# Kernel optimization log

Hardware: AMD Instinct MI355X
Metric: run time of the kernel (lower is better)

## Reference

```python
import jax, jax.numpy as jnp
import numpy as np


def _lap(cost):
    """Jonker-Volgenant / e-maxx O(n^3) Hungarian on a square numpy cost matrix.
    Returns col_of_row[r] = column optimally assigned to row r (same optimum as
    scipy.optimize.linear_sum_assignment). 1-indexed internals per the classic
    formulation; inner column scans are numpy-vectorized."""
    n = cost.shape[0]
    u = np.zeros(n + 1, dtype=np.float64)
    v = np.zeros(n + 1, dtype=np.float64)
    p = np.zeros(n + 1, dtype=np.int64)    # p[j] = row matched to column j (0 = none)
    way = np.zeros(n + 1, dtype=np.int64)
    for i in range(1, n + 1):
        p[0] = i
        j0 = 0
        minv = np.full(n + 1, np.inf)
        used = np.zeros(n + 1, dtype=bool)
        while True:
            used[j0] = True
            i0 = p[j0]
            cur = cost[i0 - 1].astype(np.float64) - u[i0] - v[1:]
            free = ~used[1:]
            mv = minv[1:]          # view into minv
            wy = way[1:]           # view into way
            better = free & (cur < mv)
            mv[better] = cur[better]
            wy[better] = j0
            cand = np.where(free, mv, np.inf)
            j1 = int(np.argmin(cand)) + 1
            delta = cand[j1 - 1]
            u[p[used]] += delta
            v[used] -= delta
            mv[free] -= delta
            j0 = j1
            if p[j0] == 0:
                break
        while j0:
            j1 = way[j0]
            p[j0] = p[j1]
            j0 = j1
    col_of_row = np.empty(n, dtype=np.int64)
    for j in range(1, n + 1):
        col_of_row[p[j] - 1] = j - 1
    return col_of_row


def setup_inputs() -> dict:
    key = jax.random.key(0)
    k1, k2 = jax.random.split(key)
    pred = jax.random.normal(k1, (32, 256, 2), dtype=jnp.float32)
    target = jax.random.normal(k2, (32, 256, 2), dtype=jnp.float32)
    return {"pred": pred, "target": target}


def reference(pred, target):
    B = pred.shape[0]
    p = pred.reshape(B, -1, 2).astype(jnp.float32)   # [B, N, 2]
    t = target.reshape(B, -1, 2).astype(jnp.float32)  # [B, N, 2]
    # batched euclidean cdist: [B, N, N]
    dist = jnp.sqrt(jnp.sum((p[:, :, None, :] - t[:, None, :, :]) ** 2, axis=-1))
    dist_np = np.asarray(dist)
    # Hungarian assignment per sample (host-side, mirroring scipy in the original).
    cols = jnp.asarray(np.stack([_lap(dist_np[i]) for i in range(B)]))  # [B, N]
    matched_t = t[jnp.arange(B)[:, None], cols]       # [B, N, 2]
    # per-sample mse then mean over batch == global mean (equal sizes)
    return jnp.mean((p - matched_t) ** 2)
```

## Files before the change

kernel.cpp:

```cpp
#include <hip/hip_runtime.h>
#include <math.h>


#define N 256

typedef double dbl2 __attribute__((ext_vector_type(2)));

static __device__ __forceinline__ int f2i(float x) { union { float f; int i; } u; u.f = x; return u.i; }
static __device__ __forceinline__ float i2f(int x) { union { float f; int i; } u; u.i = x; return u.f; }
static __device__ __forceinline__ double mkd(int lo, int hi) {
  union { unsigned long long u; double d; } w;
  w.u = (((unsigned long long)(unsigned)hi) << 32) | (unsigned)lo;
  return w.d;
}
static __device__ __forceinline__ int dlo(double d) { union { double d; unsigned long long u; } w; w.d = d; return (int)(unsigned)w.u; }
static __device__ __forceinline__ int dhi(double d) { union { double d; unsigned long long u; } w; w.d = d; return (int)(unsigned)(w.u >> 32); }

#if __has_builtin(__builtin_amdgcn_sqrtf)
#define FAST_SQRT(x) __builtin_amdgcn_sqrtf(x)
#else
#define FAST_SQRT(x) sqrtf(x)
#endif

#if __has_builtin(__builtin_amdgcn_permlane16_swap) && __has_builtin(__builtin_amdgcn_permlane32_swap)
#define HAVE_PL_SWAP 1
#else
#define HAVE_PL_SWAP 0
#endif

#define DPP_MIN_STAGE(CTRL, RMASK)                                              \
  {                                                                             \
    int mlo = dlo(bm), mhi = dhi(bm);                                           \
    int slo = __builtin_amdgcn_update_dpp(mlo, mlo, CTRL, RMASK, 0xF, false);   \
    int shi = __builtin_amdgcn_update_dpp(mhi, mhi, CTRL, RMASK, 0xF, false);   \
    bm = fmin(bm, mkd(slo, shi));                                               \
  }

struct alignas(16) UC { double u; float cx, cy; };

__global__ __launch_bounds__(64) void hung_kernel(const float* __restrict__ pred,
                                                  const float* __restrict__ target,
                                                  double* __restrict__ partial) {
  const int b = blockIdx.x;
  const int lane = threadIdx.x;

  __shared__ UC ucofc[N + 1];

  float tx[4], ty[4], rpx[4], rpy[4];
  dbl2 v01 = {0.0, 0.0}, v23 = {0.0, 0.0};
  dbl2 sv01 = {0.0, 0.0}, sv23 = {0.0, 0.0};
  dbl2 ua01 = {0.0, 0.0}, ua23 = {0.0, 0.0};

  const float2* pv = (const float2*)pred + (size_t)b * N;
  const float2* tv = (const float2*)target + (size_t)b * N;
#pragma unroll
  for (int k = 0; k < 4; ++k) {
    int idx = lane + 64 * k;
    float2 pp = pv[idx];
    rpx[k] = pp.x; rpy[k] = pp.y;
    float2 tt = tv[idx];
    tx[k] = tt.x; ty[k] = tt.y;
  }
#pragma unroll
  for (int k = 0; k < 5; ++k) {
    int j = lane + 64 * k;
    if (j < N + 1) { UC z; z.u = 0.0; z.cx = 0.f; z.cy = 0.f; ucofc[j] = z; }
  }
  __syncthreads();

  unsigned long long am0 = 0, am1 = 0, am2 = 0, am3 = 0;
  const double NINF = -__builtin_huge_val();

  for (int i = 1; i <= N; ++i) {
    double uv0 = 0.0;
    double ui0 = 0.0;
    float pxi, pyi, rix, riy;
    {
      const int rl = (i - 1) & 63, rs = (i - 1) >> 6;
      pxi = i2f(__builtin_amdgcn_readlane(
          rs == 0 ? f2i(rpx[0]) : rs == 1 ? f2i(rpx[1]) : rs == 2 ? f2i(rpx[2]) : f2i(rpx[3]), rl));
      pyi = i2f(__builtin_amdgcn_readlane(
          rs == 0 ? f2i(rpy[0]) : rs == 1 ? f2i(rpy[1]) : rs == 2 ? f2i(rpy[2]) : f2i(rpy[3]), rl));
      rix = pxi; riy = pyi;
    }

    int jfin;
    int guard = N + 2;
    while (true) {
      float dx0 = pxi - tx[0], dy0 = pyi - ty[0];
      float dx1 = pxi - tx[1], dy1 = pyi - ty[1];
      float dx2 = pxi - tx[2], dy2 = pyi - ty[2];
      float dx3 = pxi - tx[3], dy3 = pyi - ty[3];
      float c0 = FAST_SQRT(dx0 * dx0 + dy0 * dy0);
      float c1 = FAST_SQRT(dx1 * dx1 + dy1 * dy1);
      float c2 = FAST_SQRT(dx2 * dx2 + dy2 * dy2);
      float c3 = FAST_SQRT(dx3 * dx3 + dy3 * dy3);
      const dbl2 ui2 = {ui0, ui0};
      dbl2 c01 = {(double)c0, (double)c1};
      dbl2 c23 = {(double)c2, (double)c3};
      const dbl2 m01 = (c01 - ui2) - sv01;
      const dbl2 m23 = (c23 - ui2) - sv23;
      double bm = fmin(fmin(m01.x, m01.y), fmin(m23.x, m23.y));

      DPP_MIN_STAGE(0xB1, 0xF);
      DPP_MIN_STAGE(0x4E, 0xF);
      DPP_MIN_STAGE(0x141, 0xF);
      DPP_MIN_STAGE(0x140, 0xF);
#if HAVE_PL_SWAP
      {
        int mlo = dlo(bm), mhi = dhi(bm);
        auto rlo = __builtin_amdgcn_permlane16_swap(mlo, mlo, false, false);
        auto rhi = __builtin_amdgcn_permlane16_swap(mhi, mhi, false, false);
        bm = fmin(mkd(rlo[0], rhi[0]), mkd(rlo[1], rhi[1]));
      }
      {
        int mlo = dlo(bm), mhi = dhi(bm);
        auto rlo = __builtin_amdgcn_permlane32_swap(mlo, mlo, false, false);
        auto rhi = __builtin_amdgcn_permlane32_swap(mhi, mhi, false, false);
        bm = fmin(mkd(rlo[0], rhi[0]), mkd(rlo[1], rhi[1]));
      }
      const double delta = bm;
#else
      DPP_MIN_STAGE(0x142, 0xA);
      DPP_MIN_STAGE(0x143, 0xC);
      const double delta = mkd(__builtin_amdgcn_readlane(dlo(bm), 63),
                               __builtin_amdgcn_readlane(dhi(bm), 63));
#endif

      const unsigned long long b0 = __ballot(m01.x == delta);
      const unsigned long long b1 = __ballot(m01.y == delta);
      const unsigned long long b2 = __ballot(m23.x == delta);
      const unsigned long long b3 = __ballot(m23.y == delta);
      const int ks = b0 ? 0 : (b1 ? 1 : (b2 ? 2 : 3));
      const unsigned long long bb = b0 ? b0 : (b1 ? b1 : (b2 ? b2 : b3));
      const int ls = (__ffsll(bb) - 1) & 63;
      const int j1 = 1 + ls + 64 * ks;

      const UC hop = ucofc[j1];

      uv0 += delta;
      {
        const dbl2 a01 = {sv01.x == NINF ? delta : 0.0, sv01.y == NINF ? delta : 0.0};
        const dbl2 a23 = {sv23.x == NINF ? delta : 0.0, sv23.y == NINF ? delta : 0.0};
        v01 -= a01; ua01 += a01;
        v23 -= a23; ua23 += a23;
      }

      const unsigned long long am = ks == 0 ? am0 : ks == 1 ? am1 : ks == 2 ? am2 : am3;
      if (!((am >> ls) & 1) || --guard == 0) { jfin = j1; break; }

      const bool hit = (lane == ls);
      sv01.x = (hit && ks == 0) ? NINF : sv01.x;
      sv01.y = (hit && ks == 1) ? NINF : sv01.y;
      sv23.x = (hit && ks == 2) ? NINF : sv23.x;
      sv23.y = (hit && ks == 3) ? NINF : sv23.y;
      ui0 = hop.u;
      pxi = hop.cx; pyi = hop.cy;
    }

    {
      const int fl = (jfin - 1) & 63, fs = ((jfin - 1) >> 6) & 3;
      const unsigned long long bit = 1ull << fl;
      if (fs == 0) am0 |= bit; else if (fs == 1) am1 |= bit;
      else if (fs == 2) am2 |= bit; else am3 |= bit;
      const bool ahit = (lane == fl);
      ua01.x = (ahit && fs == 0) ? uv0 : ua01.x;
      ua01.y = (ahit && fs == 1) ? uv0 : ua01.y;
      ua23.x = (ahit && fs == 2) ? uv0 : ua23.x;
      ua23.y = (ahit && fs == 3) ? uv0 : ua23.y;
    }
    UC nu; nu.u = uv0; nu.cx = rix; nu.cy = riy;
    ucofc[jfin] = nu;
    ucofc[1 + lane].u       = ua01.x;
    ucofc[1 + lane + 64].u  = ua01.y;
    ucofc[1 + lane + 128].u = ua23.x;
    ucofc[1 + lane + 192].u = ua23.y;
    sv01 = v01; sv23 = v23;
    __builtin_amdgcn_wave_barrier();
  }

  __syncthreads();
  double s = 0.0;
#pragma unroll
  for (int k = 0; k < 4; ++k) {
    int j = 1 + lane + 64 * k;
    UC t = ucofc[j];
    double dx = (double)t.cx - (double)tx[k];
    double dy = (double)t.cy - (double)ty[k];
    s += dx * dx + dy * dy;
  }
#pragma unroll
  for (int off = 1; off < 64; off <<= 1) s += __shfl_xor(s, off);
  if (lane == 0) partial[b] = s;
}

__global__ __launch_bounds__(64) void reduce_kernel(const double* __restrict__ partial,
                                                    float* __restrict__ out, int B) {
  double s = 0.0;
  for (int i = threadIdx.x; i < B; i += 64) s += partial[i];
#pragma unroll
  for (int off = 1; off < 64; off <<= 1) s += __shfl_xor(s, off);
  if (threadIdx.x == 0) out[0] = (float)(s / (double)(B * N * 2));
}

extern "C" void kernel_launch(void* const* d_in, const int* in_sizes, int n_in,
                              void* d_out, int out_size, void* d_ws, size_t ws_size,
                              hipStream_t stream) {
  const float* pred = (const float*)d_in[0];
  const float* target = (const float*)d_in[1];
  float* out = (float*)d_out;
  double* partial = (double*)d_ws;

  const int B = in_sizes[0] / (N * 2);

  hipLaunchKernelGGL(hung_kernel, dim3(B), dim3(64), 0, stream, pred, target, partial);
  hipLaunchKernelGGL(reduce_kernel, dim3(1), dim3(64), 0, stream, partial, out, B);
}
```

Before: 660.4 us.

## Interleave column ownership per lane and use a single ballot for argmin lookup

```diff
diff --git a/kernel.cpp b/kernel.cpp
--- a/kernel.cpp
+++ b/kernel.cpp
@@ -36,15 +36,14 @@
     bm = fmin(bm, mkd(slo, shi));                                               \
   }
 
-struct alignas(16) UC { double u; float cx, cy; };
-
 __global__ __launch_bounds__(64) void hung_kernel(const float* __restrict__ pred,
                                                   const float* __restrict__ target,
                                                   double* __restrict__ partial) {
   const int b = blockIdx.x;
   const int lane = threadIdx.x;
 
-  __shared__ UC ucofc[N + 1];
+  __shared__ double u_lds[N];
+  __shared__ float2 c_lds[N];
 
   float tx[4], ty[4], rpx[4], rpy[4];
   dbl2 v01 = {0.0, 0.0}, v23 = {0.0, 0.0};
@@ -53,18 +52,21 @@
 
   const float2* pv = (const float2*)pred + (size_t)b * N;
   const float2* tv = (const float2*)target + (size_t)b * N;
+  {
+    float4 t01 = ((const float4*)tv)[2 * lane];
+    float4 t23 = ((const float4*)tv)[2 * lane + 1];
+    tx[0] = t01.x; ty[0] = t01.y; tx[1] = t01.z; ty[1] = t01.w;
+    tx[2] = t23.x; ty[2] = t23.y; tx[3] = t23.z; ty[3] = t23.w;
+  }
 #pragma unroll
   for (int k = 0; k < 4; ++k) {
-    int idx = lane + 64 * k;
-    float2 pp = pv[idx];
+    float2 pp = pv[lane + 64 * k];
     rpx[k] = pp.x; rpy[k] = pp.y;
-    float2 tt = tv[idx];
-    tx[k] = tt.x; ty[k] = tt.y;
-  }
-#pragma unroll
-  for (int k = 0; k < 5; ++k) {
+  }
+#pragma unroll
+  for (int k = 0; k < 4; ++k) {
     int j = lane + 64 * k;
-    if (j < N + 1) { UC z; z.u = 0.0; z.cx = 0.f; z.cy = 0.f; ucofc[j] = z; }
+    u_lds[j] = 0.0; c_lds[j] = make_float2(0.f, 0.f);
   }
   __syncthreads();
 
@@ -84,7 +86,7 @@
       rix = pxi; riy = pyi;
     }
 
-    int jfin;
+    int jfin0;
     int guard = N + 2;
     while (true) {
       float dx0 = pxi - tx[0], dy0 = pyi - ty[0];
@@ -100,8 +102,11 @@
       dbl2 c23 = {(double)c2, (double)c3};
       const dbl2 m01 = (c01 - ui2) - sv01;
       const dbl2 m23 = (c23 - ui2) - sv23;
-      double bm = fmin(fmin(m01.x, m01.y), fmin(m23.x, m23.y));
-
+      const double bml = fmin(fmin(m01.x, m01.y), fmin(m23.x, m23.y));
+
+      const int bk = (m01.x == bml) ? 0 : (m01.y == bml) ? 1 : (m23.x == bml) ? 2 : 3;
+
+      double bm = bml;
       DPP_MIN_STAGE(0xB1, 0xF);
       DPP_MIN_STAGE(0x4E, 0xF);
       DPP_MIN_STAGE(0x141, 0xF);
@@ -127,16 +132,13 @@
                                __builtin_amdgcn_readlane(dhi(bm), 63));
 #endif
 
-      const unsigned long long b0 = __ballot(m01.x == delta);
-      const unsigned long long b1 = __ballot(m01.y == delta);
-      const unsigned long long b2 = __ballot(m23.x == delta);
-      const unsigned long long b3 = __ballot(m23.y == delta);
-      const int ks = b0 ? 0 : (b1 ? 1 : (b2 ? 2 : 3));
-      const unsigned long long bb = b0 ? b0 : (b1 ? b1 : (b2 ? b2 : b3));
-      const int ls = (__ffsll(bb) - 1) & 63;
-      const int j1 = 1 + ls + 64 * ks;
-
-      const UC hop = ucofc[j1];
+      const unsigned long long L = __ballot(bml == delta);
+      const int ls = (__ffsll(L) - 1) & 63;
+      const int bks = __builtin_amdgcn_readlane(bk, ls) & 3;
+      const int j1i = 4 * ls + bks;
+
+      const double uj = u_lds[j1i];
+      const float2 cj = c_lds[j1i];
 
       uv0 += delta;
       {
@@ -146,20 +148,20 @@
         v23 -= a23; ua23 += a23;
       }
 
-      const unsigned long long am = ks == 0 ? am0 : ks == 1 ? am1 : ks == 2 ? am2 : am3;
-      if (!((am >> ls) & 1) || --guard == 0) { jfin = j1; break; }
+      const unsigned long long am = bks == 0 ? am0 : bks == 1 ? am1 : bks == 2 ? am2 : am3;
+      if (!((am >> ls) & 1) || --guard == 0) { jfin0 = j1i; break; }
 
       const bool hit = (lane == ls);
-      sv01.x = (hit && ks == 0) ? NINF : sv01.x;
-      sv01.y = (hit && ks == 1) ? NINF : sv01.y;
-      sv23.x = (hit && ks == 2) ? NINF : sv23.x;
-      sv23.y = (hit && ks == 3) ? NINF : sv23.y;
-      ui0 = hop.u;
-      pxi = hop.cx; pyi = hop.cy;
+      sv01.x = (hit && bks == 0) ? NINF : sv01.x;
+      sv01.y = (hit && bks == 1) ? NINF : sv01.y;
+      sv23.x = (hit && bks == 2) ? NINF : sv23.x;
+      sv23.y = (hit && bks == 3) ? NINF : sv23.y;
+      ui0 = uj;
+      pxi = cj.x; pyi = cj.y;
     }
 
     {
-      const int fl = (jfin - 1) & 63, fs = ((jfin - 1) >> 6) & 3;
+      const int fl = (jfin0 >> 2) & 63, fs = jfin0 & 3;
       const unsigned long long bit = 1ull << fl;
       if (fs == 0) am0 |= bit; else if (fs == 1) am1 |= bit;
       else if (fs == 2) am2 |= bit; else am3 |= bit;
@@ -169,25 +171,23 @@
       ua23.x = (ahit && fs == 2) ? uv0 : ua23.x;
       ua23.y = (ahit && fs == 3) ? uv0 : ua23.y;
     }
-    UC nu; nu.u = uv0; nu.cx = rix; nu.cy = riy;
-    ucofc[jfin] = nu;
-    ucofc[1 + lane].u       = ua01.x;
-    ucofc[1 + lane + 64].u  = ua01.y;
-    ucofc[1 + lane + 128].u = ua23.x;
-    ucofc[1 + lane + 192].u = ua23.y;
+    c_lds[jfin0] = make_float2(rix, riy);
+    *(dbl2*)&u_lds[4 * lane] = ua01;
+    *(dbl2*)&u_lds[4 * lane + 2] = ua23;
     sv01 = v01; sv23 = v23;
     __builtin_amdgcn_wave_barrier();
   }
 
   __syncthreads();
   double s = 0.0;
-#pragma unroll
-  for (int k = 0; k < 4; ++k) {
-    int j = 1 + lane + 64 * k;
-    UC t = ucofc[j];
-    double dx = (double)t.cx - (double)tx[k];
-    double dy = (double)t.cy - (double)ty[k];
-    s += dx * dx + dy * dy;
+  {
+    float4 cc01 = *(const float4*)&c_lds[4 * lane];
+    float4 cc23 = *(const float4*)&c_lds[4 * lane + 2];
+    double dx, dy;
+    dx = (double)cc01.x - (double)tx[0]; dy = (double)cc01.y - (double)ty[0]; s += dx * dx + dy * dy;
+    dx = (double)cc01.z - (double)tx[1]; dy = (double)cc01.w - (double)ty[1]; s += dx * dx + dy * dy;
+    dx = (double)cc23.x - (double)tx[2]; dy = (double)cc23.y - (double)ty[2]; s += dx * dx + dy * dy;
+    dx = (double)cc23.z - (double)tx[3]; dy = (double)cc23.w - (double)ty[3]; s += dx * dx + dy * dy;
   }
 #pragma unroll
   for (int off = 1; off < 64; off <<= 1) s += __shfl_xor(s, off);
```

Measured after the change: 649.4 us. About the same (-1.7%).
